# Performance work log

Hardware: AMD Instinct MI355X
Metric: run time of the kernel (lower is better)

Reference implementation:

```python
import jax, jax.numpy as jnp
import numpy as np
from jax import lax

B, T, D, H = 32, 512, 768, 768


def setup_inputs() -> dict:
    key = jax.random.key(0)
    ks = jax.random.split(key, 8)
    s_in = 1.0 / np.sqrt(D)
    s_h = 1.0 / np.sqrt(H)
    return {
        "x": jax.random.normal(ks[0], (B, T, D), jnp.float32),
        "Wx0": jax.random.normal(ks[1], (D, 4 * H), jnp.float32) * s_in,
        "Wh0": jax.random.normal(ks[2], (H, 4 * H), jnp.float32) * s_h,
        "b0": jnp.zeros((4 * H,), jnp.float32),
        "Wx1": jax.random.normal(ks[3], (H, 4 * H), jnp.float32) * s_h,
        "Wh1": jax.random.normal(ks[4], (H, 4 * H), jnp.float32) * s_h,
        "b1": jnp.zeros((4 * H,), jnp.float32),
        "ln_scale": jnp.ones((H,), jnp.float32),
        "ln_bias": jnp.zeros((H,), jnp.float32),
    }


def _lstm_layer(x, Wx, Wh, b):
    # x: [B, T, Din]; flax LSTMCell gate order (i, f, g, o); input proj has no bias.
    bsz = x.shape[0]
    hdim = Wh.shape[0]
    xg = jnp.einsum("btd,dg->btg", x, Wx)  # precompute input projections [B,T,4H]

    def step(carry, xg_t):
        c, h = carry
        gates = xg_t + h @ Wh + b  # [B, 4H]
        i, f, g, o = jnp.split(gates, 4, axis=-1)
        i = jax.nn.sigmoid(i)
        f = jax.nn.sigmoid(f)
        g = jnp.tanh(g)
        o = jax.nn.sigmoid(o)
        c = f * c + i * g
        h = o * jnp.tanh(c)
        return (c, h), h

    init = (jnp.zeros((bsz, hdim), x.dtype), jnp.zeros((bsz, hdim), x.dtype))
    _, hs = lax.scan(step, init, jnp.swapaxes(xg, 0, 1))  # hs: [T, B, H]
    return jnp.swapaxes(hs, 0, 1)


def _layer_norm(x, scale, bias, eps=1e-6):
    mean = jnp.mean(x, axis=-1, keepdims=True)
    var = jnp.mean(jnp.square(x - mean), axis=-1, keepdims=True)
    return (x - mean) * lax.rsqrt(var + eps) * scale + bias


def reference(x, Wx0, Wh0, b0, Wx1, Wh1, b1, ln_scale, ln_bias):
    # Dropout is identity (deterministic=True, eval mode).
    h = _lstm_layer(x, Wx0, Wh0, b0)
    h = _lstm_layer(h, Wx1, Wh1, b1)
    return _layer_norm(h, ln_scale, ln_bias)
```

## Files before the change

### kernel.cpp

```cpp
#include <hip/hip_runtime.h>
#include <stdint.h>
#include <cstdio>

typedef unsigned short u16;
typedef __attribute__((ext_vector_type(8))) __bf16 bf16x8;
typedef __attribute__((ext_vector_type(4))) float f32x4;
typedef __attribute__((ext_vector_type(4))) int i32x4;

#define AGENT __HIP_MEMORY_SCOPE_AGENT

__device__ __forceinline__ float bf2f(u16 u) {
  unsigned int x = ((unsigned int)u) << 16;
  return __builtin_bit_cast(float, x);
}
__device__ __forceinline__ u16 f2bf(float f) {
  unsigned int x = __builtin_bit_cast(unsigned int, f);
  unsigned int r = (x + 0x7fffu + ((x >> 16) & 1u)) >> 16;
  return (u16)r;
}
__device__ __forceinline__ float sigm(float x) { return 1.f / (1.f + __expf(-x)); }
__device__ __forceinline__ float tanh_f(float x) { return 1.f - 2.f / (__expf(2.f * x) + 1.f); }

__global__ __launch_bounds__(256) void k_cvt(const float* __restrict__ in, u16* __restrict__ out, int n4) {
  int i = blockIdx.x * 256 + threadIdx.x;
  if (i >= n4) return;
  float4 f = ((const float4*)in)[i];
  ushort4 o;
  o.x = f2bf(f.x); o.y = f2bf(f.y); o.z = f2bf(f.z); o.w = f2bf(f.w);
  ((ushort4*)out)[i] = o;
}

__global__ __launch_bounds__(256) void k_pack_wx(const float* __restrict__ Wx, u16* __restrict__ Bp) {
  int idx = blockIdx.x * 256 + threadIdx.x;
  if (idx >= 2359296) return;
  int j = idx & 7;
  int l = (idx >> 3) & 63;
  int t = idx >> 9;
  int kt = t % 24, nt = t / 24;
  int k = kt * 32 + (l >> 4) * 8 + j;
  int n = nt * 16 + (l & 15);
  Bp[idx] = f2bf(Wx[(size_t)k * 3072 + n]);
}

__global__ __launch_bounds__(256) void k_pack_wh(const float* __restrict__ Wh, u16* __restrict__ Wp) {
  int idx = blockIdx.x * 256 + threadIdx.x;
  if (idx >= 2359296) return;
  int j = idx & 7;
  int l = (idx >> 3) & 63;
  int t = idx >> 9;
  int kt = t % 24;
  int tmp = t / 24;
  int nt = tmp % 6, w = tmp / 6;
  int k = kt * 32 + (l >> 4) * 8 + j;
  int cc = l & 15;
  int vi = cc >> 2, q = cc & 3;
  int gcol = q * 768 + w * 24 + nt * 4 + vi;
  Wp[idx] = f2bf(Wh[(size_t)k * 3072 + gcol]);
}

__global__ __launch_bounds__(256, 2) void k_gemm(const u16* __restrict__ A, const u16* __restrict__ Bp,
                                                 u16* __restrict__ C) {
  const int bid = blockIdx.x;
  const int bm = bid & 127, bn = bid >> 7;
  const int tid = threadIdx.x, lane = tid & 63, wv = tid >> 6;
  const int wm = wv >> 1, wn = wv & 1;
  const int row0 = bm * 128 + wm * 64;
  const int col0 = bn * 128 + wn * 64;
  const int rlo = lane & 15, rhi = lane >> 4;
  f32x4 acc[4][4] = {};
  const u16* Ab = A + (size_t)(row0 + rlo) * 768 + rhi * 8;
  const u16* Bb = Bp + ((size_t)(bn * 8 + wn * 4) * 24 * 64 + lane) * 8;
#pragma unroll 2
  for (int kt = 0; kt < 24; ++kt) {
    bf16x8 a[4], b[4];
#pragma unroll
    for (int i = 0; i < 4; ++i) a[i] = *(const bf16x8*)(Ab + (size_t)i * 16 * 768 + kt * 32);
#pragma unroll
    for (int j = 0; j < 4; ++j) b[j] = *(const bf16x8*)(Bb + (size_t)j * 24 * 64 * 8 + (size_t)kt * 64 * 8);
#pragma unroll
    for (int i = 0; i < 4; ++i)
#pragma unroll
      for (int j = 0; j < 4; ++j)
        acc[i][j] = __builtin_amdgcn_mfma_f32_16x16x32_bf16(a[i], b[j], acc[i][j], 0, 0, 0);
  }
#pragma unroll
  for (int i = 0; i < 4; ++i)
#pragma unroll
    for (int j = 0; j < 4; ++j)
#pragma unroll
      for (int r = 0; r < 4; ++r) {
        int row = row0 + i * 16 + rhi * 4 + r;
        int col = col0 + j * 16 + rlo;
        C[(size_t)row * 3072 + col] = f2bf(acc[i][j][r]);
      }
}

__global__ __launch_bounds__(384) void k_rec(
    const u16* __restrict__ xg,
    const u16* __restrict__ Whp,
    const float* __restrict__ bias,
    int* hbuf,
    u16* __restrict__ hout_bf,
    float* __restrict__ hout_f,
    int layer) {
  __shared__ __align__(16) int hlds[4 * 400];
  __shared__ __align__(16) float wlds[6][68];

  const int wid = blockIdx.x, g = wid & 7, w = wid >> 3;
  const int tid = threadIdx.x, lane = tid & 63, wv = tid >> 6;

  bf16x8 bregE[12], bregO[12];
  {
    const u16* bp = Whp + (((size_t)(w * 6 + wv) * 24) * 64 + lane) * 8;
#pragma unroll
    for (int kk = 0; kk < 12; ++kk) {
      bregE[kk] = *(const bf16x8*)(bp + (size_t)(2 * kk) * 512);
      bregO[kk] = *(const bf16x8*)(bp + (size_t)(2 * kk + 1) * 512);
    }
  }

  const bool cellt = lane < 16;
  const int vi = lane & 3, r = (lane >> 2) & 3;
  const int unit = w * 24 + wv * 4 + vi;
  const int seq = g * 4 + r;
  float bv0 = 0, bv1 = 0, bv2 = 0, bv3 = 0, xv0 = 0, xv1 = 0, xv2 = 0, xv3 = 0;
  if (cellt) {
    bv0 = bias[unit]; bv1 = bias[768 + unit]; bv2 = bias[1536 + unit]; bv3 = bias[2304 + unit];
    const u16* xr = xg + (size_t)seq * 512 * 3072;
    xv0 = bf2f(xr[unit]); xv1 = bf2f(xr[768 + unit]);
    xv2 = bf2f(xr[1536 + unit]); xv3 = bf2f(xr[2304 + unit]);
  }
  float cst = 0.f;
  const int sl = (lane & 15) < 4 ? (lane & 15) : 3;
  const int abase = sl * 400 + (lane >> 4) * 4;
  const int c = tid;
  const int hrow = c / 96, hcol = (c % 96) * 4;
  int guard = 0;

  __syncthreads();

  for (int t = 0; t < 512; ++t) {
    const int expect = t;
    int* src = hbuf + (size_t)(g * 2 + (t & 1)) * 3072;
    const int* p0 = src + 8 * c;
    const int* p1 = src + 8 * c + 4;
    i32x4 v0, v1;
    for (;;) {
      asm volatile("global_load_dwordx4 %0, %2, off sc0 sc1\n\t"
                   "global_load_dwordx4 %1, %3, off sc0 sc1\n\t"
                   "s_waitcnt vmcnt(0)"
                   : "=&v"(v0), "=&v"(v1)
                   : "v"(p0), "v"(p1)
                   : "memory");
      bool ok = true;
#pragma unroll
      for (int j = 0; j < 4; ++j)
        ok = ok && ((v0[j] & 0xffff) == expect) && ((v1[j] & 0xffff) == expect);
      if (ok || ++guard > (1 << 22)) break;
    }
    __syncthreads();

    {
      int4 pk;
      pk.x = (int)(((unsigned)v0[0] >> 16) | ((unsigned)v0[1] & 0xffff0000u));
      pk.y = (int)(((unsigned)v0[2] >> 16) | ((unsigned)v0[3] & 0xffff0000u));
      pk.z = (int)(((unsigned)v1[0] >> 16) | ((unsigned)v1[1] & 0xffff0000u));
      pk.w = (int)(((unsigned)v1[2] >> 16) | ((unsigned)v1[3] & 0xffff0000u));
      *(int4*)&hlds[hrow * 400 + hcol] = pk;
    }
    __syncthreads();

    f32x4 a0 = {0, 0, 0, 0}, a1 = {0, 0, 0, 0};
#pragma unroll
    for (int kk = 0; kk < 12; ++kk) {
      bf16x8 afe = *(const bf16x8*)(hlds + abase + (2 * kk) * 16);
      bf16x8 afo = *(const bf16x8*)(hlds + abase + (2 * kk + 1) * 16);
      a0 = __builtin_amdgcn_mfma_f32_16x16x32_bf16(afe, bregE[kk], a0, 0, 0, 0);
      a1 = __builtin_amdgcn_mfma_f32_16x16x32_bf16(afo, bregO[kk], a1, 0, 0, 0);
    }
    a0 += a1;

    if (cellt) {
#pragma unroll
      for (int rr = 0; rr < 4; ++rr) wlds[wv][rr * 16 + lane] = a0[rr];
    }
    asm volatile("s_waitcnt lgkmcnt(0)" ::: "memory");
    if (cellt) {
      f32x4 tr = *(const f32x4*)&wlds[wv][r * 16 + vi * 4];
      float p0g = xv0 + tr[0] + bv0;
      float p1g = xv1 + tr[1] + bv1;
      float p2g = xv2 + tr[2] + bv2;
      float p3g = xv3 + tr[3] + bv3;
      float ig = sigm(p0g), fg = sigm(p1g), gg = tanh_f(p2g), og = sigm(p3g);
      cst = fg * cst + ig * gg;
      float h = og * tanh_f(cst);
      int* dst = hbuf + (size_t)(g * 2 + ((t + 1) & 1)) * 3072 + r * 768 + unit;
      int val = (int)(((unsigned)f2bf(h) << 16) | (unsigned)(t + 1));
      __hip_atomic_store(dst, val, __ATOMIC_RELAXED, AGENT);
      size_t o = ((size_t)seq * 512 + t) * 768 + unit;
      if (layer == 0) hout_bf[o] = f2bf(h); else hout_f[o] = h;
      if (t + 1 < 512) {
        const u16* xr = xg + ((size_t)seq * 512 + t + 1) * 3072;
        xv0 = bf2f(xr[unit]); xv1 = bf2f(xr[768 + unit]);
        xv2 = bf2f(xr[1536 + unit]); xv3 = bf2f(xr[2304 + unit]);
      }
    }
  }
}

__global__ __launch_bounds__(256) void k_ln(const float* __restrict__ in, const float* __restrict__ sc,
                                            const float* __restrict__ bi, float* __restrict__ out) {
  const int row = blockIdx.x, tid = threadIdx.x;
  const float* x = in + (size_t)row * 768;
  float v0 = x[tid], v1 = x[tid + 256], v2 = x[tid + 512];
  float s = v0 + v1 + v2;
  float s2 = v0 * v0 + v1 * v1 + v2 * v2;
#pragma unroll
  for (int off = 32; off >= 1; off >>= 1) {
    s += __shfl_xor(s, off);
    s2 += __shfl_xor(s2, off);
  }
  __shared__ float red[8];
  const int wv = tid >> 6;
  if ((tid & 63) == 0) { red[wv] = s; red[4 + wv] = s2; }
  __syncthreads();
  s = red[0] + red[1] + red[2] + red[3];
  s2 = red[4] + red[5] + red[6] + red[7];
  float mean = s * (1.f / 768.f);
  float var = s2 * (1.f / 768.f) - mean * mean;
  float rs = rsqrtf(var + 1e-6f);
  float* o = out + (size_t)row * 768;
  o[tid] = (v0 - mean) * rs * sc[tid] + bi[tid];
  o[tid + 256] = (v1 - mean) * rs * sc[tid + 256] + bi[tid + 256];
  o[tid + 512] = (v2 - mean) * rs * sc[tid + 512] + bi[tid + 512];
}

extern "C" void kernel_launch(void* const* d_in, const int* in_sizes, int n_in,
                              void* d_out, int out_size, void* d_ws, size_t ws_size,
                              hipStream_t stream) {
  const float* x   = (const float*)d_in[0];
  const float* Wx0 = (const float*)d_in[1];
  const float* Wh0 = (const float*)d_in[2];
  const float* b0  = (const float*)d_in[3];
  const float* Wx1 = (const float*)d_in[4];
  const float* Wh1 = (const float*)d_in[5];
  const float* b1  = (const float*)d_in[6];
  const float* lns = (const float*)d_in[7];
  const float* lnb = (const float*)d_in[8];
  float* out = (float*)d_out;

  char* p = (char*)d_ws;
  auto alloc = [&](size_t bytes) {
    char* r = p;
    p += (bytes + 255) & ~(size_t)255;
    return r;
  };
  u16* xg    = (u16*)alloc(16384ull * 3072 * 2);
  u16* xbf   = (u16*)alloc(16384ull * 768 * 2);
  u16* h0bf  = (u16*)alloc(16384ull * 768 * 2);
  u16* Wxp0  = (u16*)alloc(2359296ull * 2);
  u16* Wxp1  = (u16*)alloc(2359296ull * 2);
  u16* Whp0  = (u16*)alloc(2359296ull * 2);
  u16* Whp1  = (u16*)alloc(2359296ull * 2);
  char* sync0 = alloc(196608ull * 2);
  int* hbuf0 = (int*)sync0;
  int* hbuf1 = (int*)(sync0 + 196608);

  if ((size_t)(p - (char*)d_ws) > ws_size) {
    fprintf(stderr, "kernel_launch: ws too small: need %zu have %zu\n",
            (size_t)(p - (char*)d_ws), ws_size);
    return;
  }

  hipMemsetAsync(sync0, 0, 196608ull * 2, stream);
  k_cvt<<<12288, 256, 0, stream>>>(x, xbf, 3145728);
  k_pack_wx<<<9216, 256, 0, stream>>>(Wx0, Wxp0);
  k_pack_wx<<<9216, 256, 0, stream>>>(Wx1, Wxp1);
  k_pack_wh<<<9216, 256, 0, stream>>>(Wh0, Whp0);
  k_pack_wh<<<9216, 256, 0, stream>>>(Wh1, Whp1);

  k_gemm<<<3072, 256, 0, stream>>>(xbf, Wxp0, xg);
  k_rec<<<256, 384, 0, stream>>>(xg, Whp0, b0, hbuf0, h0bf, nullptr, 0);
  k_gemm<<<3072, 256, 0, stream>>>(h0bf, Wxp1, xg);
  k_rec<<<256, 384, 0, stream>>>(xg, Whp1, b1, hbuf1, nullptr, (float*)d_out, 1);
  k_ln<<<16384, 256, 0, stream>>>((const float*)d_out, lns, lnb, out);
}
```

Before: 2.167 ms.

## Double-buffer recurrent h in LDS, drop a barrier, prefetch next xg early

Double-buffers the shared-memory copy of the hidden state so each timestep needs only one workgroup barrier instead of two. A raw s_waitcnt plus s_barrier replaces __syncthreads, and s_sleep is added to the global spin-wait poll. The next step's input-projection loads are issued before the MFMA loop so their latency hides behind compute, and the MFMA chain is split into four accumulators for more instruction-level parallelism. The sleep may add wakeup latency to the cross-block handoff on the critical recurrent path.

```diff
diff --git a/kernel.cpp b/kernel.cpp
--- a/kernel.cpp
+++ b/kernel.cpp
@@ -103,7 +103,7 @@
     u16* __restrict__ hout_bf,
     float* __restrict__ hout_f,
     int layer) {
-  __shared__ __align__(16) int hlds[4 * 400];
+  __shared__ __align__(16) int hlds[2][4 * 400];
   __shared__ __align__(16) float wlds[6][68];
 
   const int wid = blockIdx.x, g = wid & 7, w = wid >> 3;
@@ -140,6 +140,7 @@
   __syncthreads();
 
   for (int t = 0; t < 512; ++t) {
+    int* hb = hlds[t & 1];
     const int expect = t;
     int* src = hbuf + (size_t)(g * 2 + (t & 1)) * 3072;
     const int* p0 = src + 8 * c;
@@ -157,28 +158,36 @@
       for (int j = 0; j < 4; ++j)
         ok = ok && ((v0[j] & 0xffff) == expect) && ((v1[j] & 0xffff) == expect);
       if (ok || ++guard > (1 << 22)) break;
-    }
-    __syncthreads();
-
+      __builtin_amdgcn_s_sleep(1);
+    }
     {
       int4 pk;
       pk.x = (int)(((unsigned)v0[0] >> 16) | ((unsigned)v0[1] & 0xffff0000u));
       pk.y = (int)(((unsigned)v0[2] >> 16) | ((unsigned)v0[3] & 0xffff0000u));
       pk.z = (int)(((unsigned)v1[0] >> 16) | ((unsigned)v1[1] & 0xffff0000u));
       pk.w = (int)(((unsigned)v1[2] >> 16) | ((unsigned)v1[3] & 0xffff0000u));
-      *(int4*)&hlds[hrow * 400 + hcol] = pk;
-    }
-    __syncthreads();
-
-    f32x4 a0 = {0, 0, 0, 0}, a1 = {0, 0, 0, 0};
-#pragma unroll
-    for (int kk = 0; kk < 12; ++kk) {
-      bf16x8 afe = *(const bf16x8*)(hlds + abase + (2 * kk) * 16);
-      bf16x8 afo = *(const bf16x8*)(hlds + abase + (2 * kk + 1) * 16);
-      a0 = __builtin_amdgcn_mfma_f32_16x16x32_bf16(afe, bregE[kk], a0, 0, 0, 0);
-      a1 = __builtin_amdgcn_mfma_f32_16x16x32_bf16(afo, bregO[kk], a1, 0, 0, 0);
-    }
-    a0 += a1;
+      *(int4*)&hb[hrow * 400 + hcol] = pk;
+    }
+    u16 n0 = 0, n1 = 0, n2 = 0, n3 = 0;
+    if (cellt && t + 1 < 512) {
+      const u16* xr = xg + ((size_t)seq * 512 + t + 1) * 3072;
+      n0 = xr[unit]; n1 = xr[768 + unit]; n2 = xr[1536 + unit]; n3 = xr[2304 + unit];
+    }
+    asm volatile("s_waitcnt lgkmcnt(0)\n\ts_barrier" ::: "memory");
+
+    f32x4 a0 = {0, 0, 0, 0}, a1 = {0, 0, 0, 0}, a2 = {0, 0, 0, 0}, a3 = {0, 0, 0, 0};
+#pragma unroll
+    for (int kk = 0; kk < 12; kk += 2) {
+      bf16x8 e0 = *(const bf16x8*)(hb + abase + (2 * kk) * 16);
+      bf16x8 o0 = *(const bf16x8*)(hb + abase + (2 * kk + 1) * 16);
+      bf16x8 e1 = *(const bf16x8*)(hb + abase + (2 * kk + 2) * 16);
+      bf16x8 o1 = *(const bf16x8*)(hb + abase + (2 * kk + 3) * 16);
+      a0 = __builtin_amdgcn_mfma_f32_16x16x32_bf16(e0, bregE[kk], a0, 0, 0, 0);
+      a1 = __builtin_amdgcn_mfma_f32_16x16x32_bf16(o0, bregO[kk], a1, 0, 0, 0);
+      a2 = __builtin_amdgcn_mfma_f32_16x16x32_bf16(e1, bregE[kk + 1], a2, 0, 0, 0);
+      a3 = __builtin_amdgcn_mfma_f32_16x16x32_bf16(o1, bregO[kk + 1], a3, 0, 0, 0);
+    }
+    a0 = (a0 + a2) + (a1 + a3);
 
     if (cellt) {
 #pragma unroll
@@ -200,9 +209,7 @@
       size_t o = ((size_t)seq * 512 + t) * 768 + unit;
       if (layer == 0) hout_bf[o] = f2bf(h); else hout_f[o] = h;
       if (t + 1 < 512) {
-        const u16* xr = xg + ((size_t)seq * 512 + t + 1) * 3072;
-        xv0 = bf2f(xr[unit]); xv1 = bf2f(xr[768 + unit]);
-        xv2 = bf2f(xr[1536 + unit]); xv3 = bf2f(xr[2304 + unit]);
+        xv0 = bf2f(n0); xv1 = bf2f(n1); xv2 = bf2f(n2); xv3 = bf2f(n3);
       }
     }
   }
```

Measured after the change: 5.490 ms. 153% more time.
